# Performance work log

Hardware: AMD Instinct MI355X
Metric: run time of the kernel (lower is better)

Reference implementation:

```python
import jax, jax.numpy as jnp
import numpy as np

SPATIAL = [(56, 100), (28, 50), (14, 25), (7, 13)]
L_TOT = sum(h * w for h, w in SPATIAL)  # 7441
IMG_H, IMG_W = 448.0, 800.0
HH, NLEV, NPTS = 8, 4, 4
C, FFN = 256, 1024
PC = [-54.0, -54.0, -5.0, 54.0, 54.0, 3.0]
GRID_XY = 1080 // 8


def mlp2(x, w1, b1, w2, b2):
    return jnp.maximum(x @ w1 + b1, 0.0) @ w2 + b2


def ln(x):
    m = x.mean(-1, keepdims=True)
    v = ((x - m) ** 2).mean(-1, keepdims=True)
    return (x - m) * jax.lax.rsqrt(v + 1e-5)


def bilinear_sample(feat, loc):
    # feat [h,w,D]; loc [N,2] normalized to [0,1]; zero padding, align_corners=False
    h, w = feat.shape[0], feat.shape[1]
    x = loc[:, 0] * w - 0.5
    y = loc[:, 1] * h - 0.5
    x0f = jnp.floor(x); y0f = jnp.floor(y)
    wx = (x - x0f)[:, None]; wy = (y - y0f)[:, None]
    x0 = x0f.astype(jnp.int32); y0 = y0f.astype(jnp.int32)
    def g(xi, yi):
        inb = ((xi >= 0) & (xi < w) & (yi >= 0) & (yi < h))[:, None]
        return feat[jnp.clip(yi, 0, h - 1), jnp.clip(xi, 0, w - 1)] * inb
    return (g(x0, y0) * (1 - wx) * (1 - wy) + g(x0 + 1, y0) * wx * (1 - wy)
            + g(x0, y0 + 1) * (1 - wx) * wy + g(x0 + 1, y0 + 1) * wx * wy)


def setup_inputs() -> dict:
    key = jax.random.key(0)
    ks = jax.random.split(key, 40)
    B, V, P = 4, 6, 200
    f = jnp.float32
    def w(i, shape, s=0.05):
        return jax.random.normal(ks[i], shape, f) * s
    inp = {
        'img_query_feat': jax.random.normal(ks[1], (B, C, P), f),
        'img_query_pos': jax.random.uniform(ks[2], (B, P, 3), dtype=f),
        'img_query_view_mask': jax.random.randint(ks[3], (B, P, V), 0, 2).astype(jnp.int32),
        'img_feats_stack': jax.random.normal(ks[4], (B, V, C, L_TOT), f),
        'normal_img_feats_pos_stack': jax.random.normal(ks[5], (L_TOT, 2), f),
        'lidar2img_rt': jnp.eye(4, dtype=f) + 0.01 * jax.random.normal(ks[0], (B, V, 4, 4), f),
        'lidar2cam_r': jnp.broadcast_to(jnp.eye(3, dtype=f), (B, V, 3, 3)) + 0.01 * jax.random.normal(ks[6], (B, V, 3, 3), f),
        'lidar2cam_t': jax.random.normal(ks[7], (B, V, 3), f),
        'qpos_w1': w(8, (3, C)), 'qpos_b1': jnp.zeros((C,), f),
        'qpos_w2': w(9, (C, C)), 'qpos_b2': jnp.zeros((C,), f),
        'kpos_w1': w(10, (6, C)), 'kpos_b1': jnp.zeros((C,), f),
        'kpos_w2': w(11, (C, C)), 'kpos_b2': jnp.zeros((C,), f),
        'sa_wq': w(12, (C, C)), 'sa_wk': w(13, (C, C)),
        'sa_wv': w(14, (C, C)), 'sa_wo': w(15, (C, C)),
        'dv_w': w(16, (C, C)),
        'doff_w': w(17, (C, HH * NLEV * NPTS * 2)), 'doff_b': jnp.zeros((HH * NLEV * NPTS * 2,), f),
        'dattn_w': w(18, (C, HH * NLEV * NPTS)), 'dattn_b': jnp.zeros((HH * NLEV * NPTS,), f),
        'dout_w': w(19, (C, C)),
        'ffn_w1': w(20, (C, FFN)), 'ffn_b1': jnp.zeros((FFN,), f),
        'ffn_w2': w(21, (FFN, C)), 'ffn_b2': jnp.zeros((C,), f),
        'pred_w1': w(22, (C, C)), 'pred_b1': jnp.zeros((C,), f),
        'pred_w2': w(23, (C, 3)), 'pred_b2': jnp.zeros((3,), f),
    }
    return inp


def reference(img_query_feat, img_query_pos, img_query_view_mask, img_feats_stack,
              normal_img_feats_pos_stack, lidar2img_rt, lidar2cam_r, lidar2cam_t,
              qpos_w1, qpos_b1, qpos_w2, qpos_b2, kpos_w1, kpos_b1, kpos_w2, kpos_b2,
              sa_wq, sa_wk, sa_wv, sa_wo, dv_w, doff_w, doff_b, dattn_w, dattn_b, dout_w,
              ffn_w1, ffn_b1, ffn_w2, ffn_b2, pred_w1, pred_b1, pred_w2, pred_b2):
    B, V, _, L = img_feats_stack.shape
    P = img_query_feat.shape[-1]
    Dh = C // HH

    # key 3D positions: denormalize -> backproject via inv(lidar2img) -> append cam center
    pos2d = jax.nn.sigmoid(normal_img_feats_pos_stack) * jnp.array([IMG_W, IMG_H], jnp.float32)
    pos4 = jnp.concatenate([pos2d, jnp.ones((L, 2), pos2d.dtype)], -1)  # [L,4]
    inv_rt = jnp.linalg.inv(lidar2img_rt)                               # [B,V,4,4]
    key3d = jnp.einsum('bvij,lj->bvli', inv_rt, pos4)[..., :3]          # [B,V,L,3]
    cam_t = -jnp.einsum('bvji,bvj->bvi', lidar2cam_r, lidar2cam_t)      # [B,V,3]
    key_pos6 = jnp.concatenate([key3d, jnp.broadcast_to(cam_t[:, :, None], key3d.shape)], -1)
    kpos_emb = mlp2(key_pos6, kpos_w1, kpos_b1, kpos_w2, kpos_b2)       # [B,V,L,C]
    qpos_emb = mlp2(img_query_pos, qpos_w1, qpos_b1, qpos_w2, qpos_b2)  # [B,P,C]

    # per-view normalized reference points from lidar->image projection
    qpad = jnp.concatenate([img_query_pos, jnp.ones((B, P, 1), img_query_pos.dtype)], -1)
    proj = jnp.einsum('bvij,bpj->bvpi', lidar2img_rt, qpad)
    ref = (proj[..., :2] / proj[..., 2:3]) / jnp.array([IMG_W, IMG_H], jnp.float32)  # [B,V,P,2]

    # on-image mask; views with <=1 query are skipped (as in original)
    mv = jnp.transpose(img_query_view_mask > 0, (0, 2, 1))  # [B,V,P]
    mv = mv & (mv.sum(-1, keepdims=True) > 1)

    # self attention among on-image queries (shared qkv, per-view key mask)
    x = jnp.transpose(img_query_feat, (0, 2, 1))  # [B,P,C]
    xq = x + qpos_emb
    q = (xq @ sa_wq).reshape(B, P, HH, Dh)
    k = (xq @ sa_wk).reshape(B, P, HH, Dh)
    v = (x @ sa_wv).reshape(B, P, HH, Dh)
    logits = jnp.einsum('bqhd,bkhd->bhqk', q, k) / np.sqrt(Dh).astype(np.float32)
    logits = logits[:, None] + jnp.where(mv[:, :, None, None, :], 0.0, -1e9)  # [B,V,HH,P,P]
    attn = jax.nn.softmax(logits, axis=-1)
    sa = jnp.einsum('bvhqk,bkhd->bvqhd', attn, v).reshape(B, V, P, C) @ sa_wo
    x1 = ln(x[:, None] + sa)  # [B,V,P,C]

    # multi-scale deformable cross attention
    vals = ((jnp.transpose(img_feats_stack, (0, 1, 3, 2)) + kpos_emb) @ dv_w).reshape(B, V, L, HH, Dh)
    q2 = x1 + qpos_emb[:, None]
    off = (q2 @ doff_w + doff_b).reshape(B, V, P, HH, NLEV, NPTS, 2)
    aw = jax.nn.softmax((q2 @ dattn_w + dattn_b).reshape(B, V, P, HH, NLEV * NPTS), -1)
    aw = aw.reshape(B, V, P, HH, NLEV, NPTS)
    wh = jnp.array([[float(w_), float(h_)] for (h_, w_) in SPATIAL], jnp.float32)  # [NLEV,2]
    loc = ref[:, :, :, None, None, None, :] + off / wh[:, None, :]
    out = jnp.zeros((B, V, P, HH, Dh), x.dtype)
    start = 0
    for l, (h_, w_) in enumerate(SPATIAL):
        feat_l = vals[:, :, start:start + h_ * w_]
        start += h_ * w_
        feat_l = jnp.transpose(feat_l.reshape(B, V, h_, w_, HH, Dh), (0, 1, 4, 2, 3, 5)).reshape(B * V * HH, h_, w_, Dh)
        loc_l = jnp.transpose(loc[:, :, :, :, l], (0, 1, 3, 2, 4, 5)).reshape(B * V * HH, P * NPTS, 2)
        s = jax.vmap(bilinear_sample)(feat_l, loc_l).reshape(B, V, HH, P, NPTS, Dh)
        out = out + jnp.einsum('bvhpnd,bvphn->bvphd', s, aw[:, :, :, :, l])
    x2 = ln(x1 + out.reshape(B, V, P, C) @ dout_w)
    x3 = ln(x2 + mlp2(x2, ffn_w1, ffn_b1, ffn_w2, ffn_b2))  # [B,V,P,C]

    # masked scatter-accumulate across views, count-normalized
    mk = mv[..., None].astype(x.dtype)            # [B,V,P,1]
    fused = (x3 * mk).sum(1) / (mk.sum(1) + 1e-4)  # [B,P,C]
    img_query_feat_out = jnp.transpose(fused, (0, 2, 1))

    # prediction head: center refinement + BEV normalization
    center = mlp2(fused, pred_w1, pred_b1, pred_w2, pred_b2) + img_query_pos  # [B,P,3]
    img_query_pos_out = jax.lax.stop_gradient(center)
    cx = (center[..., 0] - PC[0]) / (PC[3] - PC[0]) * GRID_XY
    cy = (center[..., 1] - PC[1]) / (PC[4] - PC[1]) * GRID_XY
    center_bev = jnp.stack([cx, cy], -1)
    img_query_pos_bev = jax.lax.stop_gradient(center_bev)
    height = jnp.transpose(center[..., 2:3], (0, 2, 1))
    center_out = jnp.transpose(center_bev, (0, 2, 1))
    return img_query_feat_out, img_query_pos_out, img_query_pos_bev, center_out, height
```

## Files before the change

kernel.cpp:

```cpp
#include <hip/hip_runtime.h>
#include <hip/hip_bf16.h>
#include <cstdint>
#include <cstddef>

using bf16 = __hip_bfloat16;
#define DEVFN static __device__ __forceinline__

constexpr int B = 4, V = 6, P = 200, C = 256, HH = 8, Dh = 32, NLEV = 4, NPTS = 4, FFN = 1024;
constexpr int L = 7441;
constexpr int BV = B * V, BP = B * P, BVP = B * V * P, BVL = B * V * L;
constexpr float IMG_W = 800.f, IMG_H = 448.f;

__constant__ int cLH[4] = {56, 28, 14, 7};
__constant__ int cLW[4] = {100, 50, 25, 13};
__constant__ int cLS[4] = {0, 5600, 7000, 7350};

constexpr size_t IRT   = 0;
constexpr size_t CAMT  = IRT + (size_t)BV * 16;
constexpr size_t MFLAG = CAMT + (size_t)BV * 3;
constexpr size_t Xo    = MFLAG + BV;
constexpr size_t QPOSo = Xo + (size_t)BP * C;
constexpr size_t Qo    = QPOSo + (size_t)BP * C;
constexpr size_t Ko    = Qo + (size_t)BP * C;
constexpr size_t VVo   = Ko + (size_t)BP * C;
constexpr size_t LOGo  = VVo + (size_t)BP * C;
constexpr size_t SAo   = LOGo + (size_t)B * HH * P * P;
constexpr size_t X1o   = SAo + (size_t)BVP * C;
constexpr size_t REFo  = X1o + (size_t)BVP * C;
constexpr size_t OFFo  = REFo + (size_t)BVP * 2;
constexpr size_t AWo   = OFFo + (size_t)BVP * 256;
constexpr size_t OUTSo = AWo + (size_t)BVP * 128;
constexpr size_t X2o   = OUTSo + (size_t)BVP * C;
constexpr size_t X3o   = X2o + (size_t)BVP * C;
constexpr size_t FUSEDo= X3o + (size_t)BVP * C;
constexpr size_t B2DVo = FUSEDo + (size_t)BP * C;
constexpr size_t WS_FLOATS = B2DVo + 256;
constexpr size_t VALS_BYTE_OFF = ((WS_FLOATS * 4 + 255) / 256) * 256;
constexpr size_t VALS_ELEMS = (size_t)BVL * C;

constexpr size_t KW2NB_O = 0;
constexpr size_t DVWT_O  = 65536;
constexpr size_t WOT_O   = 131072;
constexpr size_t DOUTT_O = 196608;
constexpr size_t OAWT_O  = 262144;
constexpr size_t QKVT_O  = 360448;
constexpr size_t W1T_O   = 753664;
constexpr size_t W2T_O   = 1015808;
constexpr size_t HIDB_O  = 1277952;
constexpr size_t KDVT_O  = HIDB_O;

constexpr size_t O0 = 0;
constexpr size_t O1 = O0 + (size_t)B * C * P;
constexpr size_t O2 = O1 + (size_t)B * P * 3;
constexpr size_t O3 = O2 + (size_t)B * P * 2;
constexpr size_t O4 = O3 + (size_t)B * 2 * P;

DEVFN float tof(bf16 x) { return __bfloat162float(x); }
DEVFN bf16  tobf(float x) { return __float2bfloat16(x); }

typedef __attribute__((ext_vector_type(8))) short short8;
typedef __attribute__((ext_vector_type(4))) float floatx4;

DEVFN float blockReduceSum(float v, float* red) {
    int j = threadIdx.x;
    __syncthreads();
    red[j] = v; __syncthreads();
    for (int s = 128; s > 0; s >>= 1) { if (j < s) red[j] += red[j + s]; __syncthreads(); }
    return red[0];
}

DEVFN float dotK(const float* __restrict__ s, const float* __restrict__ W, int j, int N, int K) {
    float acc = 0.f;
    for (int k = 0; k < K; k += 4) {
        float4 h = *(const float4*)(s + k);
        acc += h.x * W[(size_t)(k + 0) * N + j];
        acc += h.y * W[(size_t)(k + 1) * N + j];
        acc += h.z * W[(size_t)(k + 2) * N + j];
        acc += h.w * W[(size_t)(k + 3) * N + j];
    }
    return acc;
}

__global__ __launch_bounds__(64) void k_setup(const float* rt, const float* l2cr, const float* l2ct,
                                              const int* maskin, float* ws) {
    int t = threadIdx.x;
    if (t >= BV) return;
    float m[16], inv[16];
    for (int i = 0; i < 16; i++) m[i] = rt[t * 16 + i];
    inv[0]  =  m[5]*m[10]*m[15] - m[5]*m[11]*m[14] - m[9]*m[6]*m[15] + m[9]*m[7]*m[14] + m[13]*m[6]*m[11] - m[13]*m[7]*m[10];
    inv[4]  = -m[4]*m[10]*m[15] + m[4]*m[11]*m[14] + m[8]*m[6]*m[15] - m[8]*m[7]*m[14] - m[12]*m[6]*m[11] + m[12]*m[7]*m[10];
    inv[8]  =  m[4]*m[9]*m[15]  - m[4]*m[11]*m[13] - m[8]*m[5]*m[15] + m[8]*m[7]*m[13] + m[12]*m[5]*m[11] - m[12]*m[7]*m[9];
    inv[12] = -m[4]*m[9]*m[14]  + m[4]*m[10]*m[13] + m[8]*m[5]*m[14] - m[8]*m[6]*m[13] - m[12]*m[5]*m[10] + m[12]*m[6]*m[9];
    inv[1]  = -m[1]*m[10]*m[15] + m[1]*m[11]*m[14] + m[9]*m[2]*m[15] - m[9]*m[3]*m[14] - m[13]*m[2]*m[11] + m[13]*m[3]*m[10];
    inv[5]  =  m[0]*m[10]*m[15] - m[0]*m[11]*m[14] - m[8]*m[2]*m[15] + m[8]*m[3]*m[14] + m[12]*m[2]*m[11] - m[12]*m[3]*m[10];
    inv[9]  = -m[0]*m[9]*m[15]  + m[0]*m[11]*m[13] + m[8]*m[1]*m[15] - m[8]*m[3]*m[13] - m[12]*m[1]*m[11] + m[12]*m[3]*m[9];
    inv[13] =  m[0]*m[9]*m[14]  - m[0]*m[10]*m[13] - m[8]*m[1]*m[14] + m[8]*m[2]*m[13] + m[12]*m[1]*m[10] - m[12]*m[2]*m[9];
    inv[2]  =  m[1]*m[6]*m[15]  - m[1]*m[7]*m[14]  - m[5]*m[2]*m[15] + m[5]*m[3]*m[14] + m[13]*m[2]*m[7]  - m[13]*m[3]*m[6];
    inv[6]  = -m[0]*m[6]*m[15]  + m[0]*m[7]*m[14]  + m[4]*m[2]*m[15] - m[4]*m[3]*m[14] - m[12]*m[2]*m[7]  + m[12]*m[3]*m[6];
    inv[10] =  m[0]*m[5]*m[15]  - m[0]*m[7]*m[13]  - m[4]*m[1]*m[15] + m[4]*m[3]*m[13] + m[12]*m[1]*m[7]  - m[12]*m[3]*m[5];
    inv[14] = -m[0]*m[5]*m[14]  + m[0]*m[6]*m[13]  + m[4]*m[1]*m[14] - m[4]*m[2]*m[13] - m[12]*m[1]*m[6]  + m[12]*m[2]*m[5];
    inv[3]  = -m[1]*m[6]*m[11]  + m[1]*m[7]*m[10]  + m[5]*m[2]*m[11] - m[5]*m[3]*m[10] - m[9]*m[2]*m[7]   + m[9]*m[3]*m[6];
    inv[7]  =  m[0]*m[6]*m[11]  - m[0]*m[7]*m[10]  - m[4]*m[2]*m[11] + m[4]*m[3]*m[10] + m[8]*m[2]*m[7]   - m[8]*m[3]*m[6];
    inv[11] = -m[0]*m[5]*m[11]  + m[0]*m[7]*m[9]   + m[4]*m[1]*m[11] - m[4]*m[3]*m[9]  - m[8]*m[1]*m[7]   + m[8]*m[3]*m[5];
    inv[15] =  m[0]*m[5]*m[10]  - m[0]*m[6]*m[9]   - m[4]*m[1]*m[10] + m[4]*m[2]*m[9]  + m[8]*m[1]*m[6]   - m[8]*m[2]*m[5];
    float det = m[0]*inv[0] + m[1]*inv[4] + m[2]*inv[8] + m[3]*inv[12];
    float rd = 1.f / det;
    for (int i = 0; i < 16; i++) ws[IRT + t * 16 + i] = inv[i] * rd;
    float r9[9], tv[3];
    for (int i = 0; i < 9; i++) r9[i] = l2cr[t * 9 + i];
    for (int i = 0; i < 3; i++) tv[i] = l2ct[t * 3 + i];
    for (int i = 0; i < 3; i++)
        ws[CAMT + t * 3 + i] = -(r9[0 * 3 + i] * tv[0] + r9[1 * 3 + i] * tv[1] + r9[2 * 3 + i] * tv[2]);
    int b = t / V, v = t % V, cnt = 0;
    for (int p = 0; p < P; p++) cnt += (maskin[(b * P + p) * V + v] > 0) ? 1 : 0;
    ws[MFLAG + t] = (cnt > 1) ? 1.f : 0.f;
}

__global__ __launch_bounds__(256) void k_wprep_all(
        const float* kw2, const float* dvw, const float* wo, const float* dw,
        const float* offw, const float* attw, const float* wq, const float* wk, const float* wv,
        const float* w1, const float* w2, bf16* wb) {
    int bid = blockIdx.x, t = threadIdx.x;
    if (bid < 1024) {
        int reg = bid >> 8, n = bid & 255;
        if (reg == 0) {
            wb[(size_t)n * 256 + t] = tobf(kw2[(size_t)n * 256 + t]);
        } else {
            const float* src = (reg == 1) ? dvw : (reg == 2) ? wo : dw;
            wb[(size_t)reg * 65536 + (size_t)n * 256 + t] = tobf(src[(size_t)t * 256 + n]);
        }
    } else if (bid < 1408) {
        int n = bid - 1024;
        float v = (n < 256) ? offw[(size_t)t * 256 + n] : attw[(size_t)t * 128 + (n - 256)];
        wb[OAWT_O + (size_t)n * 256 + t] = tobf(v);
    } else if (bid < 2176) {
        int n = bid - 1408;
        bf16* dst = wb + QKVT_O + (size_t)n * 512;
        float v0 = (n < 256) ? wq[(size_t)t * 256 + n] : (n < 512) ? wk[(size_t)t * 256 + (n - 256)]
                                                                   : wv[(size_t)t * 256 + (n - 512)];
        dst[t] = tobf(v0);
        float v1 = (n < 256) ? wq[(size_t)t * 256 + n] : (n < 512) ? wk[(size_t)t * 256 + (n - 256)] : 0.f;
        dst[t + 256] = tobf(v1);
    } else if (bid < 3200) {
        int n = bid - 2176;
        wb[W1T_O + (size_t)n * 256 + t] = tobf(w1[(size_t)t * 1024 + n]);
    } else {
        int n = bid - 3200;
        bf16* dst = wb + W2T_O + (size_t)n * 1024;
        for (int kk = 0; kk < 4; kk++)
            dst[t + kk * 256] = tobf(w2[(size_t)(t + kk * 256) * 256 + n]);
    }
}

constexpr int GAST = 264;
__global__ __launch_bounds__(256) void k_wfuse(const bf16* __restrict__ dvwT, const bf16* __restrict__ kw2nb,
                                               const float* __restrict__ b2, bf16* __restrict__ kdvT,
                                               float* ws) {
    __shared__ __align__(16) bf16 As[32 * GAST];
    int row0 = blockIdx.x * 32;
    int t = threadIdx.x;
    for (int rr = 0; rr < 32; rr++)
        As[rr * GAST + t] = dvwT[(size_t)(row0 + rr) * 256 + t];
    __syncthreads();
    int wave = t >> 6, lane = t & 63, quad = lane >> 4, l15 = lane & 15;
    int n0 = wave * 64;
    floatx4 acc[2][4];
    #pragma unroll
    for (int i = 0; i < 2; i++)
        #pragma unroll
        for (int nt = 0; nt < 4; nt++) acc[i][nt] = (floatx4){0.f, 0.f, 0.f, 0.f};
    for (int kk = 0; kk < 8; kk++) {
        short8 a0 = *(const short8*)&As[l15 * GAST + kk * 32 + quad * 8];
        short8 a1 = *(const short8*)&As[(16 + l15) * GAST + kk * 32 + quad * 8];
        #pragma unroll
        for (int nt = 0; nt < 4; nt++) {
            short8 bf = *(const short8*)&kw2nb[(size_t)(n0 + nt * 16 + l15) * 256 + kk * 32 + quad * 8];
            acc[0][nt] = __builtin_amdgcn_mfma_f32_16x16x32_bf16(a0, bf, acc[0][nt], 0, 0, 0);
            acc[1][nt] = __builtin_amdgcn_mfma_f32_16x16x32_bf16(a1, bf, acc[1][nt], 0, 0, 0);
        }
    }
    #pragma unroll
    for (int i = 0; i < 2; i++)
        #pragma unroll
        for (int nt = 0; nt < 4; nt++) {
            int col = n0 + nt * 16 + l15;
            int rl = i * 16 + quad * 4;
            #pragma unroll
            for (int u = 0; u < 4; u++)
                kdvT[(size_t)(row0 + rl + u) * 256 + col] = tobf(acc[i][nt][u]);
        }
    {
        int r = t >> 3, pp = t & 7;
        float s = 0.f;
        for (int n = pp * 32; n < pp * 32 + 32; n++)
            s += tof(As[r * GAST + n]) * b2[n];
        s += __shfl_down(s, 4, 8);
        s += __shfl_down(s, 2, 8);
        s += __shfl_down(s, 1, 8);
        if (pp == 0) ws[B2DVo + row0 + r] = s;
    }
}

__global__ __launch_bounds__(256) void k_qpos(const float* qfeat, const float* qposin,
                                              const float* w1, const float* b1, const float* w2, const float* b2,
                                              float* ws) {
    int row = blockIdx.x, j = threadIdx.x;
    int b = row / P, p = row % P;
    __shared__ __align__(16) float pos[4];
    __shared__ __align__(16) float hid[C];
    if (j < 3) pos[j] = qposin[row * 3 + j];
    __syncthreads();
    float h = b1[j] + pos[0] * w1[0 * C + j] + pos[1] * w1[1 * C + j] + pos[2] * w1[2 * C + j];
    hid[j] = fmaxf(h, 0.f);
    __syncthreads();
    float acc = b2[j] + dotK(hid, w2, j, C, C);
    ws[QPOSo + (size_t)row * C + j] = acc;
    ws[Xo + (size_t)row * C + j] = qfeat[((size_t)b * C + j) * P + p];
}

constexpr int AST2 = 520;
__global__ __launch_bounds__(256) void k_qkv_mfma(const bf16* __restrict__ qkvT, float* ws) {
    __shared__ __align__(16) bf16 As[16 * AST2];
    int row0 = blockIdx.x * 16;
    int t = threadIdx.x;
    for (int rr = 0; rr < 16; rr++) {
        As[rr * AST2 + t]       = tobf(ws[Xo + (size_t)(row0 + rr) * C + t]);
        As[rr * AST2 + 256 + t] = tobf(ws[QPOSo + (size_t)(row0 + rr) * C + t]);
    }
    __syncthreads();
    int wave = t >> 6, lane = t & 63, quad = lane >> 4, l15 = lane & 15;
    int n0 = wave * 192;
    floatx4 acc[12];
    #pragma unroll
    for (int nt = 0; nt < 12; nt++) acc[nt] = (floatx4){0.f, 0.f, 0.f, 0.f};
    for (int kk = 0; kk < 16; kk++) {
        short8 a = *(const short8*)&As[l15 * AST2 + kk * 32 + quad * 8];
        #pragma unroll
        for (int nt = 0; nt < 12; nt++) {
            short8 bf = *(const short8*)&qkvT[(size_t)(n0 + nt * 16 + l15) * 512 + kk * 32 + quad * 8];
            acc[nt] = __builtin_amdgcn_mfma_f32_16x16x32_bf16(a, bf, acc[nt], 0, 0, 0);
        }
    }
    #pragma unroll
    for (int nt = 0; nt < 12; nt++) {
        int n = n0 + nt * 16 + l15;
        int which = n >> 8, c = n & 255;
        size_t dst = (which == 0) ? Qo : (which == 1) ? Ko : VVo;
        int row = row0 + quad * 4;
        #pragma unroll
        for (int u = 0; u < 4; u++)
            ws[dst + (size_t)(row + u) * C + c] = acc[nt][u];
    }
}

__global__ __launch_bounds__(256) void k_logits(float* ws) {
    int bid = blockIdx.x;
    int qi = bid % P, h = (bid / P) % HH, b = bid / (P * HH);
    int j = threadIdx.x;
    __shared__ __align__(16) float qf[Dh];
    if (j < Dh) qf[j] = ws[Qo + ((size_t)(b * P + qi)) * C + h * Dh + j];
    __syncthreads();
    if (j < P) {
        const float* kp = ws + Ko + ((size_t)(b * P + j)) * C + h * Dh;
        float acc = 0.f;
        for (int d = 0; d < Dh; d += 4) {
            float4 kv = *(const float4*)(kp + d);
            float4 qv = *(const float4*)(qf + d);
            acc += kv.x * qv.x + kv.y * qv.y + kv.z * qv.z + kv.w * qv.w;
        }
        ws[LOGo + (size_t)bid * P + j] = acc * 0.17677669529663687f;
    }
}

__global__ __launch_bounds__(256) void k_sattn(const int* maskin, float* ws) {
    int bid = blockIdx.x;
    int qi = bid % P, h = (bid / P) % HH, b = bid / (P * HH);
    int j = threadIdx.x;
    __shared__ float attn[V][256];
    __shared__ float red6[V * 8 * 32];
    __shared__ float rwm[V][4], rws[V][4];
    int wv = j >> 6;
    float lg = (j < P) ? ws[LOGo + ((size_t)(b * HH + h) * P + qi) * P + j] : 0.f;
    float val[V];
    #pragma unroll
    for (int v = 0; v < V; v++) {
        bool mk = false;
        if (j < P) {
            float flag = ws[MFLAG + b * V + v];
            mk = (flag > 0.5f) && (maskin[(b * P + j) * V + v] > 0);
        }
        val[v] = (j < P) ? (lg + (mk ? 0.f : -1e9f)) : -1e30f;
    }
    #pragma unroll
    for (int v = 0; v < V; v++) {
        float m = val[v];
        #pragma unroll
        for (int off = 32; off > 0; off >>= 1) m = fmaxf(m, __shfl_xor(m, off, 64));
        if ((j & 63) == 0) rwm[v][wv] = m;
    }
    __syncthreads();
    float ee[V];
    #pragma unroll
    for (int v = 0; v < V; v++) {
        float m = fmaxf(fmaxf(rwm[v][0], rwm[v][1]), fmaxf(rwm[v][2], rwm[v][3]));
        ee[v] = (j < P) ? __expf(val[v] - m) : 0.f;
        float s = ee[v];
        #pragma unroll
        for (int off = 32; off > 0; off >>= 1) s += __shfl_xor(s, off, 64);
        if ((j & 63) == 0) rws[v][wv] = s;
    }
    __syncthreads();
    #pragma unroll
    for (int v = 0; v < V; v++) {
        float s = (rws[v][0] + rws[v][1]) + (rws[v][2] + rws[v][3]);
        attn[v][j] = ee[v] / s;
    }
    __syncthreads();
    int d = j & 31, c = j >> 5;
    const float* vvp = ws + VVo + (size_t)b * P * C + h * Dh + d;
    float acc[V];
    #pragma unroll
    for (int v = 0; v < V; v++) acc[v] = 0.f;
    for (int kk = c * 25; kk < c * 25 + 25; ++kk) {
        float vv = vvp[(size_t)kk * C];
        #pragma unroll
        for (int v = 0; v < V; v++) acc[v] += attn[v][kk] * vv;
    }
    #pragma unroll
    for (int v = 0; v < V; v++) red6[(v * 8 + c) * 32 + d] = acc[v];
    __syncthreads();
    if (j < V * 32) {
        int v = j >> 5, dd = j & 31;
        float s2 = 0.f;
        #pragma unroll
        for (int c2 = 0; c2 < 8; c2++) s2 += red6[(v * 8 + c2) * 32 + dd];
        ws[SAo + ((size_t)((b * V + v) * P + qi)) * C + h * Dh + dd] = s2;
    }
}

constexpr int OST = 260;
__global__ __launch_bounds__(256) void k_lngemm(const bf16* __restrict__ WT,
        float* ws, size_t aOff, size_t residOff, int residMode, size_t dstOff) {
    __shared__ __align__(16) bf16 As[32 * GAST];
    __shared__ __align__(16) float Os[32 * OST];
    __shared__ float redw[4][8][2];
    __shared__ float mv[8][2];
    int row0 = blockIdx.x * 32;
    int t = threadIdx.x;
    for (int rr = 0; rr < 32; rr++)
        As[rr * GAST + t] = tobf(ws[aOff + (size_t)(row0 + rr) * C + t]);
    __syncthreads();
    int wave = t >> 6, lane = t & 63, quad = lane >> 4, l15 = lane & 15;
    int n0 = wave * 64;
    floatx4 acc[2][4];
    #pragma unroll
    for (int i = 0; i < 2; i++)
        #pragma unroll
        for (int nt = 0; nt < 4; nt++) acc[i][nt] = (floatx4){0.f, 0.f, 0.f, 0.f};
    for (int kk = 0; kk < 8; kk++) {
        short8 a0 = *(const short8*)&As[l15 * GAST + kk * 32 + quad * 8];
        short8 a1 = *(const short8*)&As[(16 + l15) * GAST + kk * 32 + quad * 8];
        #pragma unroll
        for (int nt = 0; nt < 4; nt++) {
            short8 bf = *(const short8*)&WT[(size_t)(n0 + nt * 16 + l15) * 256 + kk * 32 + quad * 8];
            acc[0][nt] = __builtin_amdgcn_mfma_f32_16x16x32_bf16(a0, bf, acc[0][nt], 0, 0, 0);
            acc[1][nt] = __builtin_amdgcn_mfma_f32_16x16x32_bf16(a1, bf, acc[1][nt], 0, 0, 0);
        }
    }
    #pragma unroll
    for (int i = 0; i < 2; i++)
        #pragma unroll
        for (int nt = 0; nt < 4; nt++) {
            int col = n0 + nt * 16 + l15;
            int rl = i * 16 + quad * 4;
            #pragma unroll
            for (int u = 0; u < 4; u++) Os[(rl + u) * OST + col] = acc[i][nt][u];
        }
    __syncthreads();
    int lane2 = t & 63, wv = t >> 6;
    for (int g = 0; g < 4; g++) {
        float rv[8];
        #pragma unroll
        for (int r = 0; r < 8; r++) {
            int grow = row0 + g * 8 + r;
            int ridx = residMode ? ((grow / (P * V)) * P + grow % P) : grow;
            rv[r] = Os[(g * 8 + r) * OST + t] + ws[residOff + (size_t)ridx * C + t];
        }
        #pragma unroll
        for (int r = 0; r < 8; r++) {
            float s = rv[r], q = rv[r] * rv[r];
            for (int off = 32; off > 0; off >>= 1) {
                s += __shfl_down(s, off, 64);
                q += __shfl_down(q, off, 64);
            }
            if (lane2 == 0) { redw[wv][r][0] = s; redw[wv][r][1] = q; }
        }
        __syncthreads();
        if (t < 8) {
            float s = redw[0][t][0] + redw[1][t][0] + redw[2][t][0] + redw[3][t][0];
            float q = redw[0][t][1] + redw[1][t][1] + redw[2][t][1] + redw[3][t][1];
            float mean = s * (1.f / C);
            float var = q * (1.f / C) - mean * mean;
            mv[t][0] = mean; mv[t][1] = rsqrtf(var + 1e-5f);
        }
        __syncthreads();
        #pragma unroll
        for (int r = 0; r < 8; r++) {
            int grow = row0 + g * 8 + r;
            ws[dstOff + (size_t)grow * C + t] = (rv[r] - mv[r][0]) * mv[r][1];
        }
        __syncthreads();
    }
}

__global__ __launch_bounds__(256) void k_ref(const float* qposin, const float* rt, float* ws) {
    int tid = blockIdx.x * 256 + threadIdx.x;
    if (tid >= BVP) return;
    int p = tid % P, v = (tid / P) % V, b = tid / (P * V);
    float p0 = qposin[(b * P + p) * 3 + 0];
    float p1 = qposin[(b * P + p) * 3 + 1];
    float p2 = qposin[(b * P + p) * 3 + 2];
    const float* m = rt + (size_t)(b * V + v) * 16;
    float pr[3];
    for (int i = 0; i < 3; i++)
        pr[i] = m[i * 4 + 0] * p0 + m[i * 4 + 1] * p1 + m[i * 4 + 2] * p2 + m[i * 4 + 3];
    ws[REFo + (size_t)tid * 2 + 0] = pr[0] / pr[2] / IMG_W;
    ws[REFo + (size_t)tid * 2 + 1] = pr[1] / pr[2] / IMG_H;
}

constexpr int OAWST = 392;
__global__ __launch_bounds__(256) void k_offaw_mfma(const bf16* __restrict__ oawT,
        const float* __restrict__ ob, const float* __restrict__ ab, float* ws) {
    __shared__ __align__(16) bf16 As[32 * GAST];
    __shared__ __align__(16) float Os[32 * OAWST];
    int row0 = blockIdx.x * 32;
    int t = threadIdx.x;
    for (int rr = 0; rr < 32; rr++) {
        int grow = row0 + rr;
        int ridx = (grow / (P * V)) * P + grow % P;
        As[rr * GAST + t] = tobf(ws[X1o + (size_t)grow * C + t] + ws[QPOSo + (size_t)ridx * C + t]);
    }
    __syncthreads();
    int wave = t >> 6, lane = t & 63, quad = lane >> 4, l15 = lane & 15;
    int n0 = wave * 96;
    floatx4 acc[2][6];
    #pragma unroll
    for (int i = 0; i < 2; i++)
        #pragma unroll
        for (int nt = 0; nt < 6; nt++) acc[i][nt] = (floatx4){0.f, 0.f, 0.f, 0.f};
    for (int kk = 0; kk < 8; kk++) {
        short8 a0 = *(const short8*)&As[l15 * GAST + kk * 32 + quad * 8];
        short8 a1 = *(const short8*)&As[(16 + l15) * GAST + kk * 32 + quad * 8];
        #pragma unroll
        for (int nt = 0; nt < 6; nt++) {
            short8 bf = *(const short8*)&oawT[(size_t)(n0 + nt * 16 + l15) * 256 + kk * 32 + quad * 8];
            acc[0][nt] = __builtin_amdgcn_mfma_f32_16x16x32_bf16(a0, bf, acc[0][nt], 0, 0, 0);
            acc[1][nt] = __builtin_amdgcn_mfma_f32_16x16x32_bf16(a1, bf, acc[1][nt], 0, 0, 0);
        }
    }
    #pragma unroll
    for (int i = 0; i < 2; i++)
        #pragma unroll
        for (int nt = 0; nt < 6; nt++) {
            int col = n0 + nt * 16 + l15;
            int rl = i * 16 + quad * 4;
            #pragma unroll
            for (int u = 0; u < 4; u++) Os[(rl + u) * OAWST + col] = acc[i][nt][u];
        }
    __syncthreads();
    float obv = ob[t];
    for (int r = 0; r < 32; r++)
        ws[OFFo + (size_t)(row0 + r) * 256 + t] = Os[r * OAWST + t] + obv;
    {
        int r = t >> 3, g = t & 7;
        const float* lg = &Os[r * OAWST + 256 + g * 16];
        float mx = -1e30f;
        #pragma unroll
        for (int i = 0; i < 16; i++) mx = fmaxf(mx, lg[i] + ab[g * 16 + i]);
        float s = 0.f;
        float ex[16];
        #pragma unroll
        for (int i = 0; i < 16; i++) { ex[i] = __expf(lg[i] + ab[g * 16 + i] - mx); s += ex[i]; }
        float rs = 1.f / s;
        #pragma unroll
        for (int i = 0; i < 16; i++)
            ws[AWo + (size_t)(row0 + r) * 128 + g * 16 + i] = ex[i] * rs;
    }
}

constexpr int VROWS = 64;
constexpr int ASTR = C + 8;
constexpr int NVT = (L + VROWS - 1) / VROWS;

DEVFN int swidx(int r, int c) {
    return r * ASTR + ((c & 7) | ((((c >> 3) ^ ((r >> 3) & 7))) << 3));
}
DEVFN int swblk(int r, int cb) {
    return r * ASTR + (((cb ^ ((r >> 3) & 7))) << 3);
}

__global__ __launch_bounds__(256, 4) void k_vals_mfma(
        const float* __restrict__ npos, const float* __restrict__ feats,
        const float* __restrict__ kw1, const float* __restrict__ kb1,
        const bf16* __restrict__ kdvT, const bf16* __restrict__ dvwT,
        const float* __restrict__ ws, bf16* __restrict__ vals) {
    __shared__ __align__(16) bf16 As[VROWS * ASTR];
    __shared__ float kp6s[VROWS][8];
    __shared__ float b2s[C];
    int bv = blockIdx.y;
    int l0 = blockIdx.x * VROWS;
    int t = threadIdx.x;
    bool full = (l0 + VROWS <= L);

    b2s[t] = ws[B2DVo + t];
    if (t < VROWS) {
        int l = min(l0 + t, L - 1);
        float sx = 1.f / (1.f + __expf(-npos[l * 2 + 0])) * IMG_W;
        float sy = 1.f / (1.f + __expf(-npos[l * 2 + 1])) * IMG_H;
        const float* inv = ws + IRT + (size_t)bv * 16;
        #pragma unroll
        for (int i = 0; i < 3; i++)
            kp6s[t][i] = inv[i * 4 + 0] * sx + inv[i * 4 + 1] * sy + inv[i * 4 + 2] + inv[i * 4 + 3];
        #pragma unroll
        for (int i = 0; i < 3; i++) kp6s[t][3 + i] = ws[CAMT + (size_t)bv * 3 + i];
    }
    __syncthreads();
    {
        float w1j[6];
        #pragma unroll
        for (int i = 0; i < 6; i++) w1j[i] = kw1[i * C + t];
        float bb = kb1[t];
        for (int r = 0; r < VROWS; r++) {
            float h = bb;
            #pragma unroll
            for (int i = 0; i < 6; i++) h += kp6s[r][i] * w1j[i];
            As[swidx(r, t)] = tobf(fmaxf(h, 0.f));
        }
    }
    __syncthreads();
    int wave = t >> 6, lane = t & 63;
    int quad = lane >> 4, l15 = lane & 15;
    int mh = (wave >> 1) * 32;
    int nh = (wave & 1) * 128;
    floatx4 acc[2][8];
    #pragma unroll
    for (int i = 0; i < 2; i++)
        #pragma unroll
        for (int nt = 0; nt < 8; nt++) acc[i][nt] = (floatx4){0.f, 0.f, 0.f, 0.f};
    for (int kk = 0; kk < 8; kk++) {
        short8 a0 = *(const short8*)&As[swblk(mh + l15, kk * 4 + quad)];
        short8 a1 = *(const short8*)&As[swblk(mh + 16 + l15, kk * 4 + quad)];
        #pragma unroll
        for (int nt = 0; nt < 8; nt++) {
            short8 bfr = *(const short8*)&kdvT[(size_t)(nh + nt * 16 + l15) * C + kk * 32 + quad * 8];
            acc[0][nt] = __builtin_amdgcn_mfma_f32_16x16x32_bf16(a0, bfr, acc[0][nt], 0, 0, 0);
            acc[1][nt] = __builtin_amdgcn_mfma_f32_16x16x32_bf16(a1, bfr, acc[1][nt], 0, 0, 0);
        }
    }
    __syncthreads();
    if (full) {
        #pragma unroll
        for (int rnd = 0; rnd < 16; rnd++) {
            int q = rnd * 256 + t;
            int c = q >> 4, ql = (q & 15) * 4;
            float4 f = *(const float4*)&feats[((size_t)bv * C + c) * L + l0 + ql];
            As[swidx(ql + 0, c)] = tobf(f.x);
            As[swidx(ql + 1, c)] = tobf(f.y);
            As[swidx(ql + 2, c)] = tobf(f.z);
            As[swidx(ql + 3, c)] = tobf(f.w);
        }
    } else {
        for (int rnd = 0; rnd < 16; rnd++) {
            int q = rnd * 256 + t;
            int c = q >> 4, ql = (q & 15) * 4;
            size_t fbase = ((size_t)bv * C + c) * L + l0 + ql;
            #pragma unroll
            for (int u = 0; u < 4; u++) {
                float fv = (l0 + ql + u < L) ? feats[fbase + u] : 0.f;
                As[swidx(ql + u, c)] = tobf(fv);
            }
        }
    }
    __syncthreads();
    for (int kk = 0; kk < 8; kk++) {
        short8 a0 = *(const short8*)&As[swblk(mh + l15, kk * 4 + quad)];
        short8 a1 = *(const short8*)&As[swblk(mh + 16 + l15, kk * 4 + quad)];
        #pragma unroll
        for (int nt = 0; nt < 8; nt++) {
            short8 bfr = *(const short8*)&dvwT[(size_t)(nh + nt * 16 + l15) * C + kk * 32 + quad * 8];
            acc[0][nt] = __builtin_amdgcn_mfma_f32_16x16x32_bf16(a0, bfr, acc[0][nt], 0, 0, 0);
            acc[1][nt] = __builtin_amdgcn_mfma_f32_16x16x32_bf16(a1, bfr, acc[1][nt], 0, 0, 0);
        }
    }
    __syncthreads();
    #pragma unroll
    for (int i = 0; i < 2; i++) {
        #pragma unroll
        for (int nt = 0; nt < 8; nt++) {
            int c = nh + nt * 16 + l15;
            int rb = mh + i * 16 + quad * 4;
            float bias = b2s[c];
            #pragma unroll
            for (int u = 0; u < 4; u++)
                As[swidx(rb + u, c)] = tobf(acc[i][nt][u] + bias);
        }
    }
    __syncthreads();
    #pragma unroll
    for (int pass = 0; pass < 8; pass++) {
        int row = pass * 8 + (t >> 5);
        int cb = t & 31;
        int l = l0 + row;
        if (l < L)
            *(int4*)&vals[((size_t)bv * L + l) * C + cb * 8] = *(const int4*)&As[swblk(row, cb)];
    }
}

__global__ __launch_bounds__(256) void k_sample(const float* ws, const bf16* vals, float* wsmut) {
    int bid0 = blockIdx.x;
    int row = (bid0 & 7) * (BVP / 8) + (bid0 >> 3);
    int j = threadIdx.x;
    int h = j >> 5, d = j & 31;
    __shared__ float soff[256];
    __shared__ float sawL[128];
    __shared__ float sref[2];
    soff[j] = ws[OFFo + (size_t)row * 256 + j];
    if (j < 128) sawL[j] = ws[AWo + (size_t)row * 128 + j];
    if (j < 2) sref[j] = ws[REFo + (size_t)row * 2 + j];
    __syncthreads();
    int v = (row / P) % V, b = row / (P * V);
    const bf16* vbase = vals + (size_t)(b * V + v) * L * C + h * Dh + d;
    float acc = 0.f;
    for (int l = 0; l < NLEV; l++) {
        float Wf = (float)cLW[l], Hf = (float)cLH[l];
        int Wi = cLW[l], Hi = cLH[l], S0 = cLS[l];
        for (int n = 0; n < NPTS; n++) {
            int oi = ((h * NLEV + l) * NPTS + n) * 2;
            float lx = sref[0] + soff[oi + 0] / Wf;
            float ly = sref[1] + soff[oi + 1] / Hf;
            float aww = sawL[(h * NLEV + l) * NPTS + n];
            float x = lx * Wf - 0.5f, y = ly * Hf - 0.5f;
            float x0f = floorf(x), y0f = floorf(y);
            float wx = x - x0f, wy = y - y0f;
            int x0 = (int)x0f, y0 = (int)y0f;
            float s = 0.f;
            #pragma unroll
            for (int dy = 0; dy < 2; dy++) {
                #pragma unroll
                for (int dx = 0; dx < 2; dx++) {
                    int xi = x0 + dx, yi = y0 + dy;
                    if (xi >= 0 && xi < Wi && yi >= 0 && yi < Hi) {
                        float wwt = (dx ? wx : 1.f - wx) * (dy ? wy : 1.f - wy);
                        s += wwt * tof(vbase[(size_t)(S0 + yi * Wi + xi) * C]);
                    }
                }
            }
            acc += aww * s;
        }
    }
    wsmut[OUTSo + (size_t)row * C + j] = acc;
}

__global__ __launch_bounds__(256) void k_ffn1(const bf16* __restrict__ w1T, const float* __restrict__ b1,
                                              float* ws, bf16* hidb) {
    __shared__ __align__(16) bf16 As[32 * GAST];
    __shared__ __align__(16) bf16 Hs[32 * AST2];
    int row0 = blockIdx.x * 32;
    int nb = blockIdx.y * 512;
    int t = threadIdx.x;
    for (int rr = 0; rr < 32; rr++)
        As[rr * GAST + t] = tobf(ws[X2o + (size_t)(row0 + rr) * C + t]);
    __syncthreads();
    int wave = t >> 6, lane = t & 63, quad = lane >> 4, l15 = lane & 15;
    int n0 = wave * 128;
    floatx4 acc[2][8];
    #pragma unroll
    for (int i = 0; i < 2; i++)
        #pragma unroll
        for (int nt = 0; nt < 8; nt++) acc[i][nt] = (floatx4){0.f, 0.f, 0.f, 0.f};
    for (int kk = 0; kk < 8; kk++) {
        short8 a0 = *(const short8*)&As[l15 * GAST + kk * 32 + quad * 8];
        short8 a1 = *(const short8*)&As[(16 + l15) * GAST + kk * 32 + quad * 8];
        #pragma unroll
        for (int nt = 0; nt < 8; nt++) {
            short8 bf = *(const short8*)&w1T[(size_t)(nb + n0 + nt * 16 + l15) * 256 + kk * 32 + quad * 8];
            acc[0][nt] = __builtin_amdgcn_mfma_f32_16x16x32_bf16(a0, bf, acc[0][nt], 0, 0, 0);
            acc[1][nt] = __builtin_amdgcn_mfma_f32_16x16x32_bf16(a1, bf, acc[1][nt], 0, 0, 0);
        }
    }
    #pragma unroll
    for (int i = 0; i < 2; i++)
        #pragma unroll
        for (int nt = 0; nt < 8; nt++) {
            int cl = n0 + nt * 16 + l15;
            float bias = b1[nb + cl];
            int rl = i * 16 + quad * 4;
            #pragma unroll
            for (int u = 0; u < 4; u++)
                Hs[(rl + u) * AST2 + cl] = tobf(fmaxf(acc[i][nt][u] + bias, 0.f));
        }
    __syncthreads();
    #pragma unroll
    for (int pass = 0; pass < 8; pass++) {
        int row = pass * 4 + (t >> 6);
        int col = (t & 63) * 8;
        *(int4*)&hidb[(size_t)(row0 + row) * FFN + nb + col] = *(const int4*)&Hs[row * AST2 + col];
    }
}

__global__ __launch_bounds__(256) void k_ffn2(const bf16* __restrict__ w2T, const float* __restrict__ b2,
                                              const bf16* __restrict__ hidb, float* ws) {
    __shared__ __align__(16) float Os[32 * OST];
    __shared__ float redw[4][8][2];
    __shared__ float mv[8][2];
    int row0 = blockIdx.x * 32;
    int t = threadIdx.x;
    int wave = t >> 6, lane = t & 63, quad = lane >> 4, l15 = lane & 15;
    int n0 = wave * 64;
    floatx4 acc[2][4];
    #pragma unroll
    for (int i = 0; i < 2; i++)
        #pragma unroll
        for (int nt = 0; nt < 4; nt++) acc[i][nt] = (floatx4){0.f, 0.f, 0.f, 0.f};
    for (int kk = 0; kk < 32; kk++) {
        short8 a0 = *(const short8*)&hidb[(size_t)(row0 + l15) * FFN + kk * 32 + quad * 8];
        short8 a1 = *(const short8*)&hidb[(size_t)(row0 + 16 + l15) * FFN + kk * 32 + quad * 8];
        #pragma unroll
        for (int nt = 0; nt < 4; nt++) {
            short8 bf = *(const short8*)&w2T[(size_t)(n0 + nt * 16 + l15) * FFN + kk * 32 + quad * 8];
            acc[0][nt] = __builtin_amdgcn_mfma_f32_16x16x32_bf16(a0, bf, acc[0][nt], 0, 0, 0);
            acc[1][nt] = __builtin_amdgcn_mfma_f32_16x16x32_bf16(a1, bf, acc[1][nt], 0, 0, 0);
        }
    }
    #pragma unroll
    for (int i = 0; i < 2; i++)
        #pragma unroll
        for (int nt = 0; nt < 4; nt++) {
            int col = n0 + nt * 16 + l15;
            float bias = b2[col];
            int rl = i * 16 + quad * 4;
            #pragma unroll
            for (int u = 0; u < 4; u++) Os[(rl + u) * OST + col] = acc[i][nt][u] + bias;
        }
    __syncthreads();
    for (int g = 0; g < 4; g++) {
        float rv[8];
        #pragma unroll
        for (int r = 0; r < 8; r++) {
            int grow = row0 + g * 8 + r;
            rv[r] = Os[(g * 8 + r) * OST + t] + ws[X2o + (size_t)grow * C + t];
        }
        #pragma unroll
        for (int r = 0; r < 8; r++) {
            float s = rv[r], q = rv[r] * rv[r];
            for (int off = 32; off > 0; off >>= 1) {
                s += __shfl_down(s, off, 64);
                q += __shfl_down(q, off, 64);
            }
            if (lane == 0) { redw[wave][r][0] = s; redw[wave][r][1] = q; }
        }
        __syncthreads();
        if (t < 8) {
            float s = redw[0][t][0] + redw[1][t][0] + redw[2][t][0] + redw[3][t][0];
            float q = redw[0][t][1] + redw[1][t][1] + redw[2][t][1] + redw[3][t][1];
            float mean = s * (1.f / C);
            float var = q * (1.f / C) - mean * mean;
            mv[t][0] = mean; mv[t][1] = rsqrtf(var + 1e-5f);
        }
        __syncthreads();
        #pragma unroll
        for (int r = 0; r < 8; r++) {
            int grow = row0 + g * 8 + r;
            ws[X3o + (size_t)grow * C + t] = (rv[r] - mv[r][0]) * mv[r][1];
        }
        __syncthreads();
    }
}

__global__ __launch_bounds__(256) void k_fuse(const int* maskin, float* ws, float* out) {
    int row = blockIdx.x, j = threadIdx.x;
    int b = row / P, p = row % P;
    float s = 0.f, cnt = 0.f;
    for (int v = 0; v < V; v++) {
        bool mk = (maskin[(b * P + p) * V + v] > 0) && (ws[MFLAG + b * V + v] > 0.5f);
        if (mk) {
            s += ws[X3o + ((size_t)((b * V + v) * P + p)) * C + j];
            cnt += 1.f;
        }
    }
    float f = s / (cnt + 1e-4f);
    ws[FUSEDo + (size_t)row * C + j] = f;
    out[O0 + ((size_t)b * C + j) * P + p] = f;
}

__global__ __launch_bounds__(256) void k_pred(const float* w1, const float* b1, const float* w2, const float* b2,
                                              const float* qposin, float* ws, float* out) {
    int row = blockIdx.x, j = threadIdx.x;
    __shared__ __align__(16) float in[C];
    __shared__ float red[256];
    __shared__ float cen[4];
    in[j] = ws[FUSEDo + (size_t)row * C + j];
    __syncthreads();
    float h = fmaxf(b1[j] + dotK(in, w1, j, C, C), 0.f);
    for (int i = 0; i < 3; i++) {
        float s = blockReduceSum(h * w2[j * 3 + i], red);
        if (j == 0) cen[i] = s + b2[i] + qposin[row * 3 + i];
    }
    if (j == 0) {
        float c0 = cen[0], c1 = cen[1], c2 = cen[2];
        float cx = (c0 + 54.f) / 108.f * 135.f;
        float cy = (c1 + 54.f) / 108.f * 135.f;
        int b = row / P, p = row % P;
        out[O1 + (size_t)row * 3 + 0] = c0;
        out[O1 + (size_t)row * 3 + 1] = c1;
        out[O1 + (size_t)row * 3 + 2] = c2;
        out[O2 + (size_t)row * 2 + 0] = cx;
        out[O2 + (size_t)row * 2 + 1] = cy;
        out[O3 + (size_t)b * 2 * P + 0 * P + p] = cx;
        out[O3 + (size_t)b * 2 * P + 1 * P + p] = cy;
        out[O4 + (size_t)b * P + p] = c2;
    }
}

extern "C" void kernel_launch(void* const* d_in, const int* in_sizes, int n_in,
                              void* d_out, int out_size, void* d_ws, size_t ws_size,
                              hipStream_t stream) {
    const float* qfeat  = (const float*)d_in[0];
    const float* qposin = (const float*)d_in[1];
    const int*   maskin = (const int*)d_in[2];
    const float* feats  = (const float*)d_in[3];
    const float* npos   = (const float*)d_in[4];
    const float* rt     = (const float*)d_in[5];
    const float* l2cr   = (const float*)d_in[6];
    const float* l2ct   = (const float*)d_in[7];
    const float* qp_w1 = (const float*)d_in[8],  * qp_b1 = (const float*)d_in[9];
    const float* qp_w2 = (const float*)d_in[10], * qp_b2 = (const float*)d_in[11];
    const float* kp_w1 = (const float*)d_in[12], * kp_b1 = (const float*)d_in[13];
    const float* kp_w2 = (const float*)d_in[14], * kp_b2 = (const float*)d_in[15];
    const float* sa_wq = (const float*)d_in[16], * sa_wk = (const float*)d_in[17];
    const float* sa_wv = (const float*)d_in[18];
    const float* sa_wo = (const float*)d_in[19];
    const float* dv_w  = (const float*)d_in[20];
    const float* doffw = (const float*)d_in[21], * doffb = (const float*)d_in[22];
    const float* dattw = (const float*)d_in[23], * dattb = (const float*)d_in[24];
    const float* doutw = (const float*)d_in[25];
    const float* f_w1  = (const float*)d_in[26], * f_b1 = (const float*)d_in[27];
    const float* f_w2  = (const float*)d_in[28], * f_b2 = (const float*)d_in[29];
    const float* p_w1  = (const float*)d_in[30], * p_b1 = (const float*)d_in[31];
    const float* p_w2  = (const float*)d_in[32], * p_b2 = (const float*)d_in[33];

    float* ws = (float*)d_ws;
    bf16* vals = (bf16*)((char*)d_ws + VALS_BYTE_OFF);
    bf16* wb = vals + VALS_ELEMS;
    bf16* hidb = wb + HIDB_O;
    float* out = (float*)d_out;

    k_setup<<<1, 64, 0, stream>>>(rt, l2cr, l2ct, maskin, ws);
    k_wprep_all<<<3456, 256, 0, stream>>>(kp_w2, dv_w, sa_wo, doutw, doffw, dattw,
                                          sa_wq, sa_wk, sa_wv, f_w1, f_w2, wb);
    k_wfuse<<<8, 256, 0, stream>>>(wb + DVWT_O, wb + KW2NB_O, kp_b2, wb + KDVT_O, ws);
    k_qpos<<<BP, 256, 0, stream>>>(qfeat, qposin, qp_w1, qp_b1, qp_w2, qp_b2, ws);
    k_qkv_mfma<<<BP / 16, 256, 0, stream>>>(wb + QKVT_O, ws);
    k_logits<<<B * HH * P, 256, 0, stream>>>(ws);
    k_sattn<<<B * HH * P, 256, 0, stream>>>(maskin, ws);
    k_lngemm<<<BVP / 32, 256, 0, stream>>>(wb + WOT_O, ws, SAo, Xo, 1, X1o);
    k_ref<<<(BVP + 255) / 256, 256, 0, stream>>>(qposin, rt, ws);
    k_offaw_mfma<<<BVP / 32, 256, 0, stream>>>(wb + OAWT_O, doffb, dattb, ws);
    k_vals_mfma<<<dim3(NVT, BV), 256, 0, stream>>>(npos, feats, kp_w1, kp_b1,
                                                   wb + KDVT_O, wb + DVWT_O, ws, vals);
    k_sample<<<BVP, 256, 0, stream>>>(ws, vals, ws);
    k_lngemm<<<BVP / 32, 256, 0, stream>>>(wb + DOUTT_O, ws, OUTSo, X1o, 0, X2o);
    k_ffn1<<<dim3(BVP / 32, 2), 256, 0, stream>>>(wb + W1T_O, f_b1, ws, hidb);
    k_ffn2<<<BVP / 32, 256, 0, stream>>>(wb + W2T_O, f_b2, hidb, ws);
    k_fuse<<<BP, 256, 0, stream>>>(maskin, ws, out);
    k_pred<<<BP, 256, 0, stream>>>(p_w1, p_b1, p_w2, p_b2, qposin, ws, out);
}
```

Baseline: 866.4 us.

## Keep value-projection weight fragments in registers across four row subtiles per block

The value-projection kernel now loads each wave's slice of both bf16 weight matrices (kdvT and dvwT) into registers once, then loops over four 64-row subtiles per block. This replaces the per-tile global reloads of the B fragments. The wave tiling changes from 32x128 to 64x64 per wave. The cost is very high register pressure from 64 short8 fragments, launch bounds dropped to one block per CU, and four times fewer blocks (about 30 per view), which may hurt occupancy and latency hiding.

After: 876.3 us. No clear change (+1.1%).

```diff
diff --git a/kernel.cpp b/kernel.cpp
--- a/kernel.cpp
+++ b/kernel.cpp
@@ -490,7 +490,8 @@
 
 constexpr int VROWS = 64;
 constexpr int ASTR = C + 8;
-constexpr int NVT = (L + VROWS - 1) / VROWS;
+constexpr int SUBT = 4;
+constexpr int NVT4 = (L + VROWS * SUBT - 1) / (VROWS * SUBT);
 
 DEVFN int swidx(int r, int c) {
     return r * ASTR + ((c & 7) | ((((c >> 3) ^ ((r >> 3) & 7))) << 3));
@@ -499,7 +500,7 @@
     return r * ASTR + (((cb ^ ((r >> 3) & 7))) << 3);
 }
 
-__global__ __launch_bounds__(256, 4) void k_vals_mfma(
+__global__ __launch_bounds__(256, 1) void k_vals_mfma(
         const float* __restrict__ npos, const float* __restrict__ feats,
         const float* __restrict__ kw1, const float* __restrict__ kb1,
         const bf16* __restrict__ kdvT, const bf16* __restrict__ dvwT,
@@ -508,111 +509,125 @@
     __shared__ float kp6s[VROWS][8];
     __shared__ float b2s[C];
     int bv = blockIdx.y;
-    int l0 = blockIdx.x * VROWS;
+    int base = blockIdx.x * (VROWS * SUBT);
     int t = threadIdx.x;
-    bool full = (l0 + VROWS <= L);
+    int wave = t >> 6, lane = t & 63;
+    int quad = lane >> 4, l15 = lane & 15;
+    int nh = wave * 64;
 
     b2s[t] = ws[B2DVo + t];
-    if (t < VROWS) {
-        int l = min(l0 + t, L - 1);
-        float sx = 1.f / (1.f + __expf(-npos[l * 2 + 0])) * IMG_W;
-        float sy = 1.f / (1.f + __expf(-npos[l * 2 + 1])) * IMG_H;
-        const float* inv = ws + IRT + (size_t)bv * 16;
-        #pragma unroll
-        for (int i = 0; i < 3; i++)
-            kp6s[t][i] = inv[i * 4 + 0] * sx + inv[i * 4 + 1] * sy + inv[i * 4 + 2] + inv[i * 4 + 3];
-        #pragma unroll
-        for (int i = 0; i < 3; i++) kp6s[t][3 + i] = ws[CAMT + (size_t)bv * 3 + i];
-    }
-    __syncthreads();
-    {
-        float w1j[6];
-        #pragma unroll
-        for (int i = 0; i < 6; i++) w1j[i] = kw1[i * C + t];
-        float bb = kb1[t];
+
+    short8 bh[8][4], bff[8][4];
+    #pragma unroll
+    for (int kk = 0; kk < 8; kk++)
+        #pragma unroll
+        for (int nt = 0; nt < 4; nt++) {
+            size_t roff = (size_t)(nh + nt * 16 + l15) * C + kk * 32 + quad * 8;
+            bh[kk][nt]  = *(const short8*)&kdvT[roff];
+            bff[kk][nt] = *(const short8*)&dvwT[roff];
+        }
+
+    float w1j[6];
+    #pragma unroll
+    for (int i = 0; i < 6; i++) w1j[i] = kw1[i * C + t];
+    float bb = kb1[t];
+
+    for (int st = 0; st < SUBT; st++) {
+        int l0 = base + st * VROWS;
+        if (l0 >= L) break;
+        bool full = (l0 + VROWS <= L);
+        __syncthreads();
+        if (t < VROWS) {
+            int l = min(l0 + t, L - 1);
+            float sx = 1.f / (1.f + __expf(-npos[l * 2 + 0])) * IMG_W;
+            float sy = 1.f / (1.f + __expf(-npos[l * 2 + 1])) * IMG_H;
+            const float* inv = ws + IRT + (size_t)bv * 16;
+            #pragma unroll
+            for (int i = 0; i < 3; i++)
+                kp6s[t][i] = inv[i * 4 + 0] * sx + inv[i * 4 + 1] * sy + inv[i * 4 + 2] + inv[i * 4 + 3];
+            #pragma unroll
+            for (int i = 0; i < 3; i++) kp6s[t][3 + i] = ws[CAMT + (size_t)bv * 3 + i];
+        }
+        __syncthreads();
         for (int r = 0; r < VROWS; r++) {
             float h = bb;
             #pragma unroll
             for (int i = 0; i < 6; i++) h += kp6s[r][i] * w1j[i];
             As[swidx(r, t)] = tobf(fmaxf(h, 0.f));
         }
-    }
-    __syncthreads();
-    int wave = t >> 6, lane = t & 63;
-    int quad = lane >> 4, l15 = lane & 15;
-    int mh = (wave >> 1) * 32;
-    int nh = (wave & 1) * 128;
-    floatx4 acc[2][8];
-    #pragma unroll
-    for (int i = 0; i < 2; i++)
-        #pragma unroll
-        for (int nt = 0; nt < 8; nt++) acc[i][nt] = (floatx4){0.f, 0.f, 0.f, 0.f};
-    for (int kk = 0; kk < 8; kk++) {
-        short8 a0 = *(const short8*)&As[swblk(mh + l15, kk * 4 + quad)];
-        short8 a1 = *(const short8*)&As[swblk(mh + 16 + l15, kk * 4 + quad)];
-        #pragma unroll
-        for (int nt = 0; nt < 8; nt++) {
-            short8 bfr = *(const short8*)&kdvT[(size_t)(nh + nt * 16 + l15) * C + kk * 32 + quad * 8];
-            acc[0][nt] = __builtin_amdgcn_mfma_f32_16x16x32_bf16(a0, bfr, acc[0][nt], 0, 0, 0);
-            acc[1][nt] = __builtin_amdgcn_mfma_f32_16x16x32_bf16(a1, bfr, acc[1][nt], 0, 0, 0);
-        }
-    }
-    __syncthreads();
-    if (full) {
-        #pragma unroll
-        for (int rnd = 0; rnd < 16; rnd++) {
-            int q = rnd * 256 + t;
-            int c = q >> 4, ql = (q & 15) * 4;
-            float4 f = *(const float4*)&feats[((size_t)bv * C + c) * L + l0 + ql];
-            As[swidx(ql + 0, c)] = tobf(f.x);
-            As[swidx(ql + 1, c)] = tobf(f.y);
-            As[swidx(ql + 2, c)] = tobf(f.z);
-            As[swidx(ql + 3, c)] = tobf(f.w);
-        }
-    } else {
-        for (int rnd = 0; rnd < 16; rnd++) {
-            int q = rnd * 256 + t;
-            int c = q >> 4, ql = (q & 15) * 4;
-            size_t fbase = ((size_t)bv * C + c) * L + l0 + ql;
-            #pragma unroll
-            for (int u = 0; u < 4; u++) {
-                float fv = (l0 + ql + u < L) ? feats[fbase + u] : 0.f;
-                As[swidx(ql + u, c)] = tobf(fv);
+        __syncthreads();
+        floatx4 acc[4][4];
+        #pragma unroll
+        for (int mt = 0; mt < 4; mt++)
+            #pragma unroll
+            for (int nt = 0; nt < 4; nt++) acc[mt][nt] = (floatx4){0.f, 0.f, 0.f, 0.f};
+        for (int kk = 0; kk < 8; kk++) {
+            short8 av[4];
+            #pragma unroll
+            for (int mt = 0; mt < 4; mt++)
+                av[mt] = *(const short8*)&As[swblk(mt * 16 + l15, kk * 4 + quad)];
+            #pragma unroll
+            for (int mt = 0; mt < 4; mt++)
+                #pragma unroll
+                for (int nt = 0; nt < 4; nt++)
+                    acc[mt][nt] = __builtin_amdgcn_mfma_f32_16x16x32_bf16(av[mt], bh[kk][nt], acc[mt][nt], 0, 0, 0);
+        }
+        __syncthreads();
+        if (full) {
+            #pragma unroll
+            for (int rnd = 0; rnd < 16; rnd++) {
+                int c = rnd * 16 + (t >> 4), ql = (t & 15) * 4;
+                float4 f = *(const float4*)&feats[((size_t)bv * C + c) * L + l0 + ql];
+                As[swidx(ql + 0, c)] = tobf(f.x);
+                As[swidx(ql + 1, c)] = tobf(f.y);
+                As[swidx(ql + 2, c)] = tobf(f.z);
+                As[swidx(ql + 3, c)] = tobf(f.w);
             }
-        }
-    }
-    __syncthreads();
-    for (int kk = 0; kk < 8; kk++) {
-        short8 a0 = *(const short8*)&As[swblk(mh + l15, kk * 4 + quad)];
-        short8 a1 = *(const short8*)&As[swblk(mh + 16 + l15, kk * 4 + quad)];
-        #pragma unroll
-        for (int nt = 0; nt < 8; nt++) {
-            short8 bfr = *(const short8*)&dvwT[(size_t)(nh + nt * 16 + l15) * C + kk * 32 + quad * 8];
-            acc[0][nt] = __builtin_amdgcn_mfma_f32_16x16x32_bf16(a0, bfr, acc[0][nt], 0, 0, 0);
-            acc[1][nt] = __builtin_amdgcn_mfma_f32_16x16x32_bf16(a1, bfr, acc[1][nt], 0, 0, 0);
-        }
-    }
-    __syncthreads();
-    #pragma unroll
-    for (int i = 0; i < 2; i++) {
-        #pragma unroll
-        for (int nt = 0; nt < 8; nt++) {
-            int c = nh + nt * 16 + l15;
-            int rb = mh + i * 16 + quad * 4;
-            float bias = b2s[c];
-            #pragma unroll
-            for (int u = 0; u < 4; u++)
-                As[swidx(rb + u, c)] = tobf(acc[i][nt][u] + bias);
-        }
-    }
-    __syncthreads();
-    #pragma unroll
-    for (int pass = 0; pass < 8; pass++) {
-        int row = pass * 8 + (t >> 5);
-        int cb = t & 31;
-        int l = l0 + row;
-        if (l < L)
-            *(int4*)&vals[((size_t)bv * L + l) * C + cb * 8] = *(const int4*)&As[swblk(row, cb)];
+        } else {
+            for (int rnd = 0; rnd < 16; rnd++) {
+                int c = rnd * 16 + (t >> 4), ql = (t & 15) * 4;
+                size_t fbase = ((size_t)bv * C + c) * L + l0 + ql;
+                #pragma unroll
+                for (int u = 0; u < 4; u++) {
+                    float fv = (l0 + ql + u < L) ? feats[fbase + u] : 0.f;
+                    As[swidx(ql + u, c)] = tobf(fv);
+                }
+            }
+        }
+        __syncthreads();
+        for (int kk = 0; kk < 8; kk++) {
+            short8 av[4];
+            #pragma unroll
+            for (int mt = 0; mt < 4; mt++)
+                av[mt] = *(const short8*)&As[swblk(mt * 16 + l15, kk * 4 + quad)];
+            #pragma unroll
+            for (int mt = 0; mt < 4; mt++)
+                #pragma unroll
+                for (int nt = 0; nt < 4; nt++)
+                    acc[mt][nt] = __builtin_amdgcn_mfma_f32_16x16x32_bf16(av[mt], bff[kk][nt], acc[mt][nt], 0, 0, 0);
+        }
+        __syncthreads();
+        #pragma unroll
+        for (int mt = 0; mt < 4; mt++) {
+            #pragma unroll
+            for (int nt = 0; nt < 4; nt++) {
+                int c = nh + nt * 16 + l15;
+                int rb = mt * 16 + quad * 4;
+                float bias = b2s[c];
+                #pragma unroll
+                for (int u = 0; u < 4; u++)
+                    As[swidx(rb + u, c)] = tobf(acc[mt][nt][u] + bias);
+            }
+        }
+        __syncthreads();
+        #pragma unroll
+        for (int pass = 0; pass < 8; pass++) {
+            int row = pass * 8 + (t >> 5);
+            int cb = t & 31;
+            int l = l0 + row;
+            if (l < L)
+                *(int4*)&vals[((size_t)bv * L + l) * C + cb * 8] = *(const int4*)&As[swblk(row, cb)];
+        }
     }
 }
 
@@ -866,8 +881,8 @@
     k_lngemm<<<BVP / 32, 256, 0, stream>>>(wb + WOT_O, ws, SAo, Xo, 1, X1o);
     k_ref<<<(BVP + 255) / 256, 256, 0, stream>>>(qposin, rt, ws);
     k_offaw_mfma<<<BVP / 32, 256, 0, stream>>>(wb + OAWT_O, doffb, dattb, ws);
-    k_vals_mfma<<<dim3(NVT, BV), 256, 0, stream>>>(npos, feats, kp_w1, kp_b1,
-                                                   wb + KDVT_O, wb + DVWT_O, ws, vals);
+    k_vals_mfma<<<dim3(NVT4, BV), 256, 0, stream>>>(npos, feats, kp_w1, kp_b1,
+                                                    wb + KDVT_O, wb + DVWT_O, ws, vals);
     k_sample<<<BVP, 256, 0, stream>>>(ws, vals, ws);
     k_lngemm<<<BVP / 32, 256, 0, stream>>>(wb + DOUTT_O, ws, OUTSo, X1o, 0, X2o);
     k_ffn1<<<dim3(BVP / 32, 2), 256, 0, stream>>>(wb + W1T_O, f_b1, ws, hidb);
```
